# Optimization experiments

Measured on AMD Instinct MI355X. Metric: run time of the kernel, lower is better.

The kernel has to match this reference:

```python
import jax, jax.numpy as jnp
import numpy as np

SM_SCALE = 0.07216878364870322  # 1/sqrt(192)
PAGE_SIZE = 64


def setup_inputs() -> dict:
    key = jax.random.key(0)
    ks = jax.random.split(key, 6)
    B, Hq, Hkv = 32, 16, 1
    DN, DR, DV = 128, 64, 128
    NUM_PAGES, MAX_PAGES = 2048, 64
    return {
        "q": jax.random.normal(ks[0], (B, Hq, DN + DR), dtype=jnp.float32),
        "k_nope_buffer": jax.random.normal(ks[1], (NUM_PAGES, PAGE_SIZE, Hkv, DN), dtype=jnp.float32),
        "k_rope_buffer": jax.random.normal(ks[2], (NUM_PAGES, PAGE_SIZE, Hkv, DR), dtype=jnp.float32),
        "v_buffer": jax.random.normal(ks[3], (NUM_PAGES, PAGE_SIZE, Hkv, DV), dtype=jnp.float32),
        "seq_lens": jax.random.randint(ks[4], (B,), 1, MAX_PAGES * PAGE_SIZE + 1, dtype=jnp.int32),
        "block_table": jax.random.randint(ks[5], (B, MAX_PAGES), 0, NUM_PAGES, dtype=jnp.int32),
    }


def reference(q, k_nope_buffer, k_rope_buffer, v_buffer, seq_lens, block_table):
    B, Hq, _ = q.shape
    Hkv = k_nope_buffer.shape[2]
    dn = k_nope_buffer.shape[-1]
    dv = v_buffer.shape[-1]
    max_kv = block_table.shape[1] * PAGE_SIZE

    q_nope = q[:, :, :dn]            # (B, Hq, dn)
    q_rope = q[:, :, dn:]            # (B, Hq, dr)

    # Gather pages per batch: (B, max_pages, page, Hkv, d) -> (B, max_kv, Hkv, d)
    kn = k_nope_buffer[block_table].reshape(B, max_kv, Hkv, dn)
    kr = k_rope_buffer[block_table].reshape(B, max_kv, Hkv, -1)
    v = v_buffer[block_table].reshape(B, max_kv, Hkv, dv)

    rep = Hq // Hkv  # GQA repeat_interleave == repeat along head axis
    if rep != 1:
        kn = jnp.repeat(kn, rep, axis=2)
        kr = jnp.repeat(kr, rep, axis=2)
        v = jnp.repeat(v, rep, axis=2)

    scores = (jnp.einsum('bhd,bkhd->bhk', q_nope, kn)
              + jnp.einsum('bhd,bkhd->bhk', q_rope, kr)).astype(jnp.float32) * SM_SCALE
    # Mask out key positions beyond each sequence length (replaces per-batch slicing)
    valid = jnp.arange(max_kv)[None, None, :] < seq_lens[:, None, None]
    scores = jnp.where(valid, scores, -jnp.inf)
    probs = jax.nn.softmax(scores, axis=-1).astype(v.dtype)  # (B, Hq, max_kv)
    out = jnp.einsum('bhk,bkhd->bhd', probs, v)              # (B, Hq, dv)
    return out
```

## Files before the change

kernel.cpp:

```cpp
#include <hip/hip_runtime.h>
#include <math.h>

#define NB 32
#define HQ 16
#define DN 128
#define DR 64
#define DQT 192
#define DV 128
#define PAGE 64
#define MAXP 64
#define NSPLIT 16
#define SPLIT_PAGES 4
#define SPLIT_T (SPLIT_PAGES * PAGE)
#define SM_SCALE 0.07216878364870322f

__global__ __launch_bounds__(256, 2)
void attn_partial_kernel(const float* __restrict__ q,
                         const float* __restrict__ kn,
                         const float* __restrict__ kr,
                         const float* __restrict__ v,
                         const int* __restrict__ seq_lens,
                         const int* __restrict__ block_table,
                         float* __restrict__ o_part,
                         float* __restrict__ ml_part)
{
    const int split = blockIdx.x;
    const int b = blockIdx.y;
    const int seq = seq_lens[b];
    const int t0 = split * SPLIT_T;
    if (t0 >= seq) return;

    const int tid = (int)threadIdx.x;
    const int wave = tid >> 6;
    const int lane = tid & 63;

    __shared__ float q_s[HQ * DQT];
    __shared__ float p_s[SPLIT_T][HQ];
    __shared__ float redmax_s[SPLIT_PAGES][HQ];
    __shared__ float redsum_s[SPLIT_PAGES][HQ];
    __shared__ float acc_s[DV][HQ + 1];
    __shared__ int bt_s[SPLIT_PAGES];

    {
        const float4* qb = (const float4*)(q + (size_t)b * HQ * DQT);
        float4* qs4 = (float4*)q_s;
        #pragma unroll
        for (int i = 0; i < 3; i++) qs4[tid + 256 * i] = qb[tid + 256 * i];
    }
    if (tid < SPLIT_PAGES)
        bt_s[tid] = block_table[b * MAXP + split * SPLIT_PAGES + tid];
    __syncthreads();

    float s[HQ];
    #pragma unroll
    for (int h = 0; h < HQ; h++) s[h] = 0.f;

    const int pbase = t0 + wave * PAGE;
    const bool wave_valid = pbase < seq;
    const bool valid = (pbase + lane) < seq;

    if (wave_valid) {
        const int pid = bt_s[wave];
        const float4* knp = (const float4*)(kn + ((size_t)pid * PAGE + lane) * DN);
        #pragma unroll 8
        for (int c = 0; c < DN / 4; c++) {
            float4 k4 = knp[c];
            #pragma unroll
            for (int h = 0; h < HQ; h++) {
                float4 q4 = ((const float4*)(q_s + h * DQT))[c];
                s[h] += q4.x * k4.x + q4.y * k4.y + q4.z * k4.z + q4.w * k4.w;
            }
        }
        const float4* krp = (const float4*)(kr + ((size_t)pid * PAGE + lane) * DR);
        #pragma unroll 8
        for (int c = 0; c < DR / 4; c++) {
            float4 k4 = krp[c];
            #pragma unroll
            for (int h = 0; h < HQ; h++) {
                float4 q4 = ((const float4*)(q_s + h * DQT))[DN / 4 + c];
                s[h] += q4.x * k4.x + q4.y * k4.y + q4.z * k4.z + q4.w * k4.w;
            }
        }
    }
    #pragma unroll
    for (int h = 0; h < HQ; h++) s[h] = valid ? s[h] * SM_SCALE : -INFINITY;

    #pragma unroll
    for (int h = 0; h < HQ; h++) {
        float m = s[h];
        #pragma unroll
        for (int off = 32; off > 0; off >>= 1) m = fmaxf(m, __shfl_xor(m, off));
        if (lane == 0) redmax_s[wave][h] = m;
    }
    __syncthreads();

    #pragma unroll
    for (int h = 0; h < HQ; h++) {
        float m = fmaxf(fmaxf(redmax_s[0][h], redmax_s[1][h]),
                        fmaxf(redmax_s[2][h], redmax_s[3][h]));
        s[h] = __expf(s[h] - m);
    }
    {
        const int t = wave * PAGE + lane;
        float4* prow = (float4*)(&p_s[t][0]);
        #pragma unroll
        for (int j = 0; j < 4; j++) {
            float4 pv;
            pv.x = s[4 * j + 0]; pv.y = s[4 * j + 1];
            pv.z = s[4 * j + 2]; pv.w = s[4 * j + 3];
            prow[j] = pv;
        }
    }
    #pragma unroll
    for (int h = 0; h < HQ; h++) {
        float l = s[h];
        #pragma unroll
        for (int off = 32; off > 0; off >>= 1) l += __shfl_xor(l, off);
        if (lane == 0) redsum_s[wave][h] = l;
    }
    __syncthreads();

    if (tid < HQ) {
        const int h = tid;
        float m = fmaxf(fmaxf(redmax_s[0][h], redmax_s[1][h]),
                        fmaxf(redmax_s[2][h], redmax_s[3][h]));
        float l = redsum_s[0][h] + redsum_s[1][h] + redsum_s[2][h] + redsum_s[3][h];
        float* ml = ml_part + ((size_t)(b * NSPLIT + split) * HQ + h) * 2;
        ml[0] = m;
        ml[1] = l;
    }

    const int g = tid >> 7;
    const int d = tid & 127;
    float acc[HQ];
    #pragma unroll
    for (int h = 0; h < HQ; h++) acc[h] = 0.f;

    #pragma unroll
    for (int w = 0; w < SPLIT_PAGES; w++) {
        const int base = w * PAGE;
        if (t0 + base >= seq) break;
        const int pid = bt_s[w];
        int rem = seq - t0 - base;
        const int lim = rem < PAGE ? rem : PAGE;
        const float* vp = v + (size_t)pid * PAGE * DV + d;
        #pragma unroll 4
        for (int l2 = g; l2 < lim; l2 += 2) {
            float vv = vp[(size_t)l2 * DV];
            const float4* prow = (const float4*)(&p_s[base + l2][0]);
            #pragma unroll
            for (int j = 0; j < 4; j++) {
                float4 p4 = prow[j];
                acc[4 * j + 0] += p4.x * vv;
                acc[4 * j + 1] += p4.y * vv;
                acc[4 * j + 2] += p4.z * vv;
                acc[4 * j + 3] += p4.w * vv;
            }
        }
    }

    if (g == 1) {
        #pragma unroll
        for (int h = 0; h < HQ; h++) acc_s[d][h] = acc[h];
    }
    __syncthreads();
    if (g == 0) {
        float* op = o_part + ((size_t)(b * NSPLIT + split) * HQ) * DV + d;
        #pragma unroll
        for (int h = 0; h < HQ; h++)
            op[h * DV] = acc[h] + acc_s[d][h];
    }
}

__global__ __launch_bounds__(128)
void attn_combine_kernel(const float* __restrict__ o_part,
                         const float* __restrict__ ml_part,
                         const int* __restrict__ seq_lens,
                         float* __restrict__ out)
{
    const int h = blockIdx.x;
    const int b = blockIdx.y;
    const int d = (int)threadIdx.x;
    const int seq = seq_lens[b];
    int ns = (seq + SPLIT_T - 1) / SPLIT_T;
    if (ns > NSPLIT) ns = NSPLIT;

    float M = -INFINITY, den = 0.f, acc = 0.f;
    for (int s2 = 0; s2 < ns; s2++) {
        const float* ml = ml_part + ((size_t)(b * NSPLIT + s2) * HQ + h) * 2;
        float m = ml[0], l = ml[1];
        float o = o_part[((size_t)(b * NSPLIT + s2) * HQ + h) * DV + d];
        float nM = fmaxf(M, m);
        float eo = __expf(M - nM);
        float en = __expf(m - nM);
        acc = acc * eo + o * en;
        den = den * eo + l * en;
        M = nM;
    }
    out[((size_t)b * HQ + h) * DV + d] = acc / den;
}

extern "C" void kernel_launch(void* const* d_in, const int* in_sizes, int n_in,
                              void* d_out, int out_size, void* d_ws, size_t ws_size,
                              hipStream_t stream)
{
    const float* q  = (const float*)d_in[0];
    const float* kn = (const float*)d_in[1];
    const float* kr = (const float*)d_in[2];
    const float* v  = (const float*)d_in[3];
    const int* seq_lens    = (const int*)d_in[4];
    const int* block_table = (const int*)d_in[5];

    float* o_part  = (float*)d_ws;
    float* ml_part = o_part + (size_t)NB * NSPLIT * HQ * DV;

    attn_partial_kernel<<<dim3(NSPLIT, NB), 256, 0, stream>>>(
        q, kn, kr, v, seq_lens, block_table, o_part, ml_part);
    attn_combine_kernel<<<dim3(HQ, NB), 128, 0, stream>>>(
        o_part, ml_part, seq_lens, (float*)d_out);
}
```

Baseline: 205.9 us.

## Rewrite split-KV attention with fp16 MFMA, per-wave online softmax, strided page splits

Replaces the scalar FP32 dot-product partial kernel with one where each wave handles its own strided set of pages. Each wave converts Q, K and V to fp16 and computes QK^T and PV with 16x16x32 MFMA instructions, keeping an online softmax across pages. The number of splits grows to 32 when workspace permits, and the combine kernel switches to a two-pass max-then-sum. This targets the FP32 ALU cost and the block-level synchronisation, at the cost of fp16 rounding of inputs and probabilities and uncoalesced strided V loads.

```diff
diff --git a/kernel.cpp b/kernel.cpp
--- a/kernel.cpp
+++ b/kernel.cpp
@@ -5,15 +5,22 @@
 #define HQ 16
 #define DN 128
 #define DR 64
-#define DQT 192
+#define DQ (DN + DR)
 #define DV 128
 #define PAGE 64
 #define MAXP 64
-#define NSPLIT 16
-#define SPLIT_PAGES 4
-#define SPLIT_T (SPLIT_PAGES * PAGE)
 #define SM_SCALE 0.07216878364870322f
-
+#define RS 88
+
+typedef __attribute__((ext_vector_type(8))) _Float16 f16x8;
+typedef __attribute__((ext_vector_type(4))) _Float16 f16x4;
+typedef __attribute__((ext_vector_type(2))) __fp16   h16x2;
+typedef __attribute__((ext_vector_type(4))) float    f32x4;
+
+union F16x8 { f16x8 v; h16x2 h[4]; };
+union F16x4 { f16x4 v; h16x2 h[2]; };
+
+template<int NSC>
 __global__ __launch_bounds__(256, 2)
 void attn_partial_kernel(const float* __restrict__ q,
                          const float* __restrict__ kn,
@@ -24,154 +31,138 @@
                          float* __restrict__ o_part,
                          float* __restrict__ ml_part)
 {
-    const int split = blockIdx.x;
-    const int b = blockIdx.y;
-    const int seq = seq_lens[b];
-    const int t0 = split * SPLIT_T;
-    if (t0 >= seq) return;
-
-    const int tid = (int)threadIdx.x;
+    const int tid  = (int)threadIdx.x;
     const int wave = tid >> 6;
     const int lane = tid & 63;
-
-    __shared__ float q_s[HQ * DQT];
-    __shared__ float p_s[SPLIT_T][HQ];
-    __shared__ float redmax_s[SPLIT_PAGES][HQ];
-    __shared__ float redsum_s[SPLIT_PAGES][HQ];
-    __shared__ float acc_s[DV][HQ + 1];
-    __shared__ int bt_s[SPLIT_PAGES];
-
+    const int ln   = lane & 15;
+    const int qd   = lane >> 4;
+
+    const int item = blockIdx.x * 4 + wave;
+    const int b = item / NSC;
+    const int c = item % NSC;
+
+    const int seq = seq_lens[b];
+    if (c * PAGE >= seq) return;
+
+    __shared__ _Float16 p_s[4][HQ][RS];
+
+    F16x8 bq[6];
     {
-        const float4* qb = (const float4*)(q + (size_t)b * HQ * DQT);
-        float4* qs4 = (float4*)q_s;
-        #pragma unroll
-        for (int i = 0; i < 3; i++) qs4[tid + 256 * i] = qb[tid + 256 * i];
-    }
-    if (tid < SPLIT_PAGES)
-        bt_s[tid] = block_table[b * MAXP + split * SPLIT_PAGES + tid];
-    __syncthreads();
-
-    float s[HQ];
+        const float* qrow = q + ((size_t)b * HQ + ln) * DQ + qd * 8;
+        #pragma unroll
+        for (int kt = 0; kt < 6; kt++) {
+            float4 x0 = *(const float4*)(qrow + kt * 32);
+            float4 x1 = *(const float4*)(qrow + kt * 32 + 4);
+            bq[kt].h[0] = __builtin_amdgcn_cvt_pkrtz(x0.x, x0.y);
+            bq[kt].h[1] = __builtin_amdgcn_cvt_pkrtz(x0.z, x0.w);
+            bq[kt].h[2] = __builtin_amdgcn_cvt_pkrtz(x1.x, x1.y);
+            bq[kt].h[3] = __builtin_amdgcn_cvt_pkrtz(x1.z, x1.w);
+        }
+    }
+
+    float m_run = -INFINITY, l_run = 0.f;
+    f32x4 o_acc[8];
     #pragma unroll
-    for (int h = 0; h < HQ; h++) s[h] = 0.f;
-
-    const int pbase = t0 + wave * PAGE;
-    const bool wave_valid = pbase < seq;
-    const bool valid = (pbase + lane) < seq;
-
-    if (wave_valid) {
-        const int pid = bt_s[wave];
-        const float4* knp = (const float4*)(kn + ((size_t)pid * PAGE + lane) * DN);
-        #pragma unroll 8
-        for (int c = 0; c < DN / 4; c++) {
-            float4 k4 = knp[c];
-            #pragma unroll
-            for (int h = 0; h < HQ; h++) {
-                float4 q4 = ((const float4*)(q_s + h * DQT))[c];
-                s[h] += q4.x * k4.x + q4.y * k4.y + q4.z * k4.z + q4.w * k4.w;
-            }
-        }
-        const float4* krp = (const float4*)(kr + ((size_t)pid * PAGE + lane) * DR);
-        #pragma unroll 8
-        for (int c = 0; c < DR / 4; c++) {
-            float4 k4 = krp[c];
-            #pragma unroll
-            for (int h = 0; h < HQ; h++) {
-                float4 q4 = ((const float4*)(q_s + h * DQT))[DN / 4 + c];
-                s[h] += q4.x * k4.x + q4.y * k4.y + q4.z * k4.z + q4.w * k4.w;
-            }
-        }
-    }
+    for (int i = 0; i < 8; i++) o_acc[i] = (f32x4){0.f, 0.f, 0.f, 0.f};
+
     #pragma unroll
-    for (int h = 0; h < HQ; h++) s[h] = valid ? s[h] * SM_SCALE : -INFINITY;
-
+    for (int pg = 0; pg < MAXP / NSC; pg++) {
+        const int page = c + pg * NSC;
+        if (page * PAGE >= seq) break;
+        const int pid = block_table[b * MAXP + page];
+
+        f32x4 sc[4];
+        #pragma unroll
+        for (int mt = 0; mt < 4; mt++) sc[mt] = (f32x4){0.f, 0.f, 0.f, 0.f};
+        const float* knb = kn + (size_t)pid * PAGE * DN;
+        const float* krb = kr + (size_t)pid * PAGE * DR;
+        #pragma unroll
+        for (int mt = 0; mt < 4; mt++) {
+            const float* rn = knb + (mt * 16 + ln) * DN + qd * 8;
+            const float* rr = krb + (mt * 16 + ln) * DR + qd * 8;
+            #pragma unroll
+            for (int kt = 0; kt < 6; kt++) {
+                const float* src = (kt < 4) ? (rn + kt * 32) : (rr + (kt - 4) * 32);
+                float4 x0 = *(const float4*)(src);
+                float4 x1 = *(const float4*)(src + 4);
+                F16x8 a;
+                a.h[0] = __builtin_amdgcn_cvt_pkrtz(x0.x, x0.y);
+                a.h[1] = __builtin_amdgcn_cvt_pkrtz(x0.z, x0.w);
+                a.h[2] = __builtin_amdgcn_cvt_pkrtz(x1.x, x1.y);
+                a.h[3] = __builtin_amdgcn_cvt_pkrtz(x1.z, x1.w);
+                sc[mt] = __builtin_amdgcn_mfma_f32_16x16x32_f16(a.v, bq[kt].v, sc[mt], 0, 0, 0);
+            }
+        }
+
+        float sv[4][4];
+        float smax = -INFINITY;
+        #pragma unroll
+        for (int mt = 0; mt < 4; mt++)
+            #pragma unroll
+            for (int r = 0; r < 4; r++) {
+                int tok = page * PAGE + mt * 16 + qd * 4 + r;
+                float x = (tok < seq) ? sc[mt][r] * SM_SCALE : -INFINITY;
+                sv[mt][r] = x;
+                smax = fmaxf(smax, x);
+            }
+        smax = fmaxf(smax, __shfl_xor(smax, 16));
+        smax = fmaxf(smax, __shfl_xor(smax, 32));
+        const float m_new = fmaxf(m_run, smax);
+        const float alpha = __expf(m_run - m_new);
+        m_run = m_new;
+        float lsum = 0.f;
+        #pragma unroll
+        for (int mt = 0; mt < 4; mt++)
+            #pragma unroll
+            for (int r = 0; r < 4; r++) {
+                float e = __expf(sv[mt][r] - m_new);
+                sv[mt][r] = e;
+                lsum += e;
+            }
+        lsum += __shfl_xor(lsum, 16);
+        lsum += __shfl_xor(lsum, 32);
+        l_run = l_run * alpha + lsum;
+
+        #pragma unroll
+        for (int mt = 0; mt < 4; mt++) {
+            F16x4 w;
+            w.h[0] = __builtin_amdgcn_cvt_pkrtz(sv[mt][0], sv[mt][1]);
+            w.h[1] = __builtin_amdgcn_cvt_pkrtz(sv[mt][2], sv[mt][3]);
+            *(f16x4*)(&p_s[wave][ln][mt * 16 + qd * 4]) = w.v;
+        }
+
+        #pragma unroll
+        for (int i = 0; i < 8; i++) o_acc[i] *= alpha;
+
+        const float* vb = v + (size_t)pid * PAGE * DV;
+        #pragma unroll
+        for (int kt2 = 0; kt2 < 2; kt2++) {
+            f16x8 pf = *(const f16x8*)(&p_s[wave][ln][kt2 * 32 + qd * 8]);
+            const int t0 = kt2 * 32 + qd * 8;
+            #pragma unroll
+            for (int mt2 = 0; mt2 < 8; mt2++) {
+                const float* vc = vb + mt2 * 16 + ln;
+                F16x8 a;
+                a.h[0] = __builtin_amdgcn_cvt_pkrtz(vc[(t0 + 0) * DV], vc[(t0 + 1) * DV]);
+                a.h[1] = __builtin_amdgcn_cvt_pkrtz(vc[(t0 + 2) * DV], vc[(t0 + 3) * DV]);
+                a.h[2] = __builtin_amdgcn_cvt_pkrtz(vc[(t0 + 4) * DV], vc[(t0 + 5) * DV]);
+                a.h[3] = __builtin_amdgcn_cvt_pkrtz(vc[(t0 + 6) * DV], vc[(t0 + 7) * DV]);
+                o_acc[mt2] = __builtin_amdgcn_mfma_f32_16x16x32_f16(a.v, pf, o_acc[mt2], 0, 0, 0);
+            }
+        }
+    }
+
+    float* op = o_part + ((size_t)(b * NSC + c) * HQ + ln) * DV + qd * 4;
     #pragma unroll
-    for (int h = 0; h < HQ; h++) {
-        float m = s[h];
-        #pragma unroll
-        for (int off = 32; off > 0; off >>= 1) m = fmaxf(m, __shfl_xor(m, off));
-        if (lane == 0) redmax_s[wave][h] = m;
-    }
-    __syncthreads();
-
-    #pragma unroll
-    for (int h = 0; h < HQ; h++) {
-        float m = fmaxf(fmaxf(redmax_s[0][h], redmax_s[1][h]),
-                        fmaxf(redmax_s[2][h], redmax_s[3][h]));
-        s[h] = __expf(s[h] - m);
-    }
-    {
-        const int t = wave * PAGE + lane;
-        float4* prow = (float4*)(&p_s[t][0]);
-        #pragma unroll
-        for (int j = 0; j < 4; j++) {
-            float4 pv;
-            pv.x = s[4 * j + 0]; pv.y = s[4 * j + 1];
-            pv.z = s[4 * j + 2]; pv.w = s[4 * j + 3];
-            prow[j] = pv;
-        }
-    }
-    #pragma unroll
-    for (int h = 0; h < HQ; h++) {
-        float l = s[h];
-        #pragma unroll
-        for (int off = 32; off > 0; off >>= 1) l += __shfl_xor(l, off);
-        if (lane == 0) redsum_s[wave][h] = l;
-    }
-    __syncthreads();
-
-    if (tid < HQ) {
-        const int h = tid;
-        float m = fmaxf(fmaxf(redmax_s[0][h], redmax_s[1][h]),
-                        fmaxf(redmax_s[2][h], redmax_s[3][h]));
-        float l = redsum_s[0][h] + redsum_s[1][h] + redsum_s[2][h] + redsum_s[3][h];
-        float* ml = ml_part + ((size_t)(b * NSPLIT + split) * HQ + h) * 2;
-        ml[0] = m;
-        ml[1] = l;
-    }
-
-    const int g = tid >> 7;
-    const int d = tid & 127;
-    float acc[HQ];
-    #pragma unroll
-    for (int h = 0; h < HQ; h++) acc[h] = 0.f;
-
-    #pragma unroll
-    for (int w = 0; w < SPLIT_PAGES; w++) {
-        const int base = w * PAGE;
-        if (t0 + base >= seq) break;
-        const int pid = bt_s[w];
-        int rem = seq - t0 - base;
-        const int lim = rem < PAGE ? rem : PAGE;
-        const float* vp = v + (size_t)pid * PAGE * DV + d;
-        #pragma unroll 4
-        for (int l2 = g; l2 < lim; l2 += 2) {
-            float vv = vp[(size_t)l2 * DV];
-            const float4* prow = (const float4*)(&p_s[base + l2][0]);
-            #pragma unroll
-            for (int j = 0; j < 4; j++) {
-                float4 p4 = prow[j];
-                acc[4 * j + 0] += p4.x * vv;
-                acc[4 * j + 1] += p4.y * vv;
-                acc[4 * j + 2] += p4.z * vv;
-                acc[4 * j + 3] += p4.w * vv;
-            }
-        }
-    }
-
-    if (g == 1) {
-        #pragma unroll
-        for (int h = 0; h < HQ; h++) acc_s[d][h] = acc[h];
-    }
-    __syncthreads();
-    if (g == 0) {
-        float* op = o_part + ((size_t)(b * NSPLIT + split) * HQ) * DV + d;
-        #pragma unroll
-        for (int h = 0; h < HQ; h++)
-            op[h * DV] = acc[h] + acc_s[d][h];
+    for (int mt2 = 0; mt2 < 8; mt2++)
+        *(f32x4*)(op + mt2 * 16) = o_acc[mt2];
+    if (qd == 0) {
+        float2* ml = (float2*)(ml_part) + (size_t)(b * NSC + c) * HQ + ln;
+        *ml = make_float2(m_run, l_run);
     }
 }
 
+template<int NSC>
 __global__ __launch_bounds__(128)
 void attn_combine_kernel(const float* __restrict__ o_part,
                          const float* __restrict__ ml_part,
@@ -182,20 +173,23 @@
     const int b = blockIdx.y;
     const int d = (int)threadIdx.x;
     const int seq = seq_lens[b];
-    int ns = (seq + SPLIT_T - 1) / SPLIT_T;
-    if (ns > NSPLIT) ns = NSPLIT;
-
-    float M = -INFINITY, den = 0.f, acc = 0.f;
+    int npages = (seq + PAGE - 1) / PAGE;
+    int ns = npages < NSC ? npages : NSC;
+
+    const float2* mlb = (const float2*)(ml_part) + (size_t)b * NSC * HQ + h;
+    float M = -INFINITY;
+    #pragma unroll 8
+    for (int s2 = 0; s2 < ns; s2++)
+        M = fmaxf(M, mlb[(size_t)s2 * HQ].x);
+
+    float acc = 0.f, den = 0.f;
+    #pragma unroll 4
     for (int s2 = 0; s2 < ns; s2++) {
-        const float* ml = ml_part + ((size_t)(b * NSPLIT + s2) * HQ + h) * 2;
-        float m = ml[0], l = ml[1];
-        float o = o_part[((size_t)(b * NSPLIT + s2) * HQ + h) * DV + d];
-        float nM = fmaxf(M, m);
-        float eo = __expf(M - nM);
-        float en = __expf(m - nM);
-        acc = acc * eo + o * en;
-        den = den * eo + l * en;
-        M = nM;
+        float2 ml = mlb[(size_t)s2 * HQ];
+        float e = __expf(ml.x - M);
+        float o = o_part[((size_t)(b * NSC + s2) * HQ + h) * DV + d];
+        acc += e * o;
+        den += e * ml.y;
     }
     out[((size_t)b * HQ + h) * DV + d] = acc / den;
 }
@@ -211,11 +205,22 @@
     const int* seq_lens    = (const int*)d_in[4];
     const int* block_table = (const int*)d_in[5];
 
-    float* o_part  = (float*)d_ws;
-    float* ml_part = o_part + (size_t)NB * NSPLIT * HQ * DV;
-
-    attn_partial_kernel<<<dim3(NSPLIT, NB), 256, 0, stream>>>(
-        q, kn, kr, v, seq_lens, block_table, o_part, ml_part);
-    attn_combine_kernel<<<dim3(HQ, NB), 128, 0, stream>>>(
-        o_part, ml_part, seq_lens, (float*)d_out);
+    const size_t need32 = (size_t)NB * 32 * HQ * (DV + 2) * 4;
+    if (ws_size >= need32) {
+        constexpr int NSC = 32;
+        float* o_part  = (float*)d_ws;
+        float* ml_part = o_part + (size_t)NB * NSC * HQ * DV;
+        attn_partial_kernel<NSC><<<NB * NSC / 4, 256, 0, stream>>>(
+            q, kn, kr, v, seq_lens, block_table, o_part, ml_part);
+        attn_combine_kernel<NSC><<<dim3(HQ, NB), 128, 0, stream>>>(
+            o_part, ml_part, seq_lens, (float*)d_out);
+    } else {
+        constexpr int NSC = 16;
+        float* o_part  = (float*)d_ws;
+        float* ml_part = o_part + (size_t)NB * NSC * HQ * DV;
+        attn_partial_kernel<NSC><<<NB * NSC / 4, 256, 0, stream>>>(
+            q, kn, kr, v, seq_lens, block_table, o_part, ml_part);
+        attn_combine_kernel<NSC><<<dim3(HQ, NB), 128, 0, stream>>>(
+            o_part, ml_part, seq_lens, (float*)d_out);
+    }
 }
```

Result: slower. 216.9 us (+5.3%).
